# Kernel optimization log

Hardware: AMD Instinct MI355X
Metric: run time of the kernel (lower is better)

The kernel has to match this reference:

```python
import jax, jax.numpy as jnp
import numpy as np

N, E, H, L, T = 20000, 160000, 128, 4, 20


def _ln(x, g, b):
    m = jnp.mean(x, -1, keepdims=True)
    v = jnp.mean((x - m) ** 2, -1, keepdims=True)
    return (x - m) * jax.lax.rsqrt(v + 1e-5) * g + b


def _mlp(x, W1, b1, W2, b2, g, b):
    # Linear -> ReLU -> Linear -> LayerNorm, as in mlp_2layer
    h = jax.nn.relu(x @ W1 + b1)
    return _ln(h @ W2 + b2, g, b)


def setup_inputs() -> dict:
    key = jax.random.key(0)
    ks = iter(jax.random.split(key, 64))

    def W(shape):
        fan_in = shape[-2]
        return jax.random.normal(next(ks), shape, jnp.float32) * (fan_in ** -0.5)

    z = lambda s: jnp.zeros(s, jnp.float32)
    o = lambda s: jnp.ones(s, jnp.float32)

    inp = {
        'x': jax.random.normal(next(ks), (N, 12), jnp.float32),
        'edge_attr': jax.random.normal(next(ks), (E, 4), jnp.float32),
        'edge_index': jax.random.randint(next(ks), (2, E), 0, N),
        # node encoder (12 -> H)
        'Wn1': W((12, H)), 'bn1': z((H,)), 'Wn2': W((H, H)), 'bn2': z((H,)), 'gn_ln': o((H,)), 'bn_ln': z((H,)),
        # edge encoder (4 -> H)
        'We1': W((4, H)), 'be1': z((H,)), 'We2': W((H, H)), 'be2': z((H,)), 'ge_ln': o((H,)), 'be_ln': z((H,)),
        # stacked per-layer params: edge_mlp (4H -> H), node_mlp (3H -> H), global_mlp (3H -> H)
        'lEW1': W((L, 4 * H, H)), 'lEb1': z((L, H)), 'lEW2': W((L, H, H)), 'lEb2': z((L, H)), 'lEg': o((L, H)), 'lEbt': z((L, H)),
        'lVW1': W((L, 3 * H, H)), 'lVb1': z((L, H)), 'lVW2': W((L, H, H)), 'lVb2': z((L, H)), 'lVg': o((L, H)), 'lVbt': z((L, H)),
        'lGW1': W((L, 3 * H, H)), 'lGb1': z((L, H)), 'lGW2': W((L, H, H)), 'lGb2': z((L, H)), 'lGg': o((L, H)), 'lGbt': z((L, H)),
        # CNN output head: Conv1d(1->8,k=15,s=4) -> ReLU -> Conv1d(8->1,k=10,s=1)
        'c1w': jax.random.normal(next(ks), (8, 1, 15), jnp.float32) * 0.1, 'c1b': z((8,)),
        'c2w': jax.random.normal(next(ks), (1, 8, 10), jnp.float32) * 0.1, 'c2b': z((1,)),
    }
    return inp


def _forward(x, edge_attr, edge_index,
             Wn1, bn1, Wn2, bn2, gn_ln, bn_ln,
             We1, be1, We2, be2, ge_ln, be_ln,
             lEW1, lEb1, lEW2, lEb2, lEg, lEbt,
             lVW1, lVb1, lVW2, lVb2, lVg, lVbt,
             lGW1, lGb1, lGW2, lGb2, lGg, lGbt,
             c1w, c1b, c2w, c2b):
    senders = edge_index[0]
    receivers = edge_index[1]
    n_nodes = x.shape[0]
    n_edges = edge_attr.shape[0]

    x_v = _mlp(x, Wn1, bn1, Wn2, bn2, gn_ln, bn_ln)          # [N, H]
    x_e = _mlp(edge_attr, We1, be1, We2, be2, ge_ln, be_ln)  # [E, H]
    g = jnp.zeros((1, H), x_v.dtype)                          # B=1 global (no global inputs)

    def step(carry, p):
        x_v, x_e, g = carry
        (EW1, Eb1, EW2, Eb2, Eg, Ebt,
         VW1, Vb1, VW2, Vb2, Vg, Vbt,
         GW1, Gb1, GW2, Gb2, Gg, Gbt) = p
        # edge update: gather sender/receiver feats, concat with edge + global
        g_e = jnp.broadcast_to(g, (n_edges, H))
        edge_in = jnp.concatenate([x_v[senders], x_v[receivers], x_e, g_e], -1)  # [E, 4H]
        x_e = x_e + _mlp(edge_in, EW1, Eb1, EW2, Eb2, Eg, Ebt)
        # node update: sum-aggregate messages by receiver
        aggr = jax.ops.segment_sum(x_e, receivers, num_segments=n_nodes)  # [N, H]
        g_v = jnp.broadcast_to(g, (n_nodes, H))
        node_in = jnp.concatenate([x_v, aggr, g_v], -1)  # [N, 3H]
        x_v = x_v + _mlp(node_in, VW1, Vb1, VW2, Vb2, Vg, Vbt)
        # global update
        g_in = jnp.concatenate([jnp.sum(x_v, 0, keepdims=True), jnp.sum(x_e, 0, keepdims=True), g], -1)  # [1, 3H]
        g = g + _mlp(g_in, GW1, Gb1, GW2, Gb2, Gg, Gbt)
        return (x_v, x_e, g), None

    params = (lEW1, lEb1, lEW2, lEb2, lEg, lEbt,
              lVW1, lVb1, lVW2, lVb2, lVg, lVbt,
              lGW1, lGb1, lGW2, lGb2, lGg, lGbt)
    (x_v, x_e, g), _ = jax.lax.scan(step, (x_v, x_e, g), params)

    # CNN head over the H=128 feature axis -> [N, T]
    dn = ('NCH', 'OIH', 'NCH')
    h = x_v[:, None, :]  # [N, 1, 128]
    h = jax.lax.conv_general_dilated(h, c1w, (4,), 'VALID', dimension_numbers=dn)
    h = jax.nn.relu(h + c1b[None, :, None])  # [N, 8, 29]
    h = jax.lax.conv_general_dilated(h, c2w, (1,), 'VALID', dimension_numbers=dn) + c2b[None, :, None]
    return h[:, 0, :]  # [N, 20]


def reference(x, edge_attr, edge_index,
              Wn1, bn1, Wn2, bn2, gn_ln, bn_ln,
              We1, be1, We2, be2, ge_ln, be_ln,
              lEW1, lEb1, lEW2, lEb2, lEg, lEbt,
              lVW1, lVb1, lVW2, lVb2, lVg, lVbt,
              lGW1, lGb1, lGW2, lGb2, lGg, lGbt,
              c1w, c1b, c2w, c2b):
    return _forward(x, edge_attr, edge_index,
                    Wn1, bn1, Wn2, bn2, gn_ln, bn_ln,
                    We1, be1, We2, be2, ge_ln, be_ln,
                    lEW1, lEb1, lEW2, lEb2, lEg, lEbt,
                    lVW1, lVb1, lVW2, lVb2, lVg, lVbt,
                    lGW1, lGb1, lGW2, lGb2, lGg, lGbt,
                    c1w, c1b, c2w, c2b)
```

## Files before the change

kernel.cpp:

```cpp
#include <hip/hip_runtime.h>

#define NN 20000
#define NE 160000
#define HD 128
#define SA 136

typedef __attribute__((ext_vector_type(8))) short  bfrag;
typedef __attribute__((ext_vector_type(4))) short  s4v;
typedef __attribute__((ext_vector_type(4))) float  facc;
typedef __attribute__((ext_vector_type(4))) float  f4v;

__device__ __forceinline__ float bf2f(unsigned short u){
  union { unsigned int i; float f; } v; v.i = ((unsigned int)u) << 16; return v.f;
}
__device__ __forceinline__ unsigned short f2bf(float f){
  union { float f; unsigned int i; } v; v.f = f;
  unsigned int r = v.i + 0x7fffu + ((v.i >> 16) & 1u);
  return (unsigned short)(r >> 16);
}

__global__ void sentinel_kernel(float* out, float code){
  if (threadIdx.x < 32) out[threadIdx.x] = code;
}

__device__ __forceinline__ void gemm_tile(const short* Ab,
                                          const unsigned short* pk,
                                          int m0, int lane, facc acc[8]){
  const int q = lane >> 4, c = lane & 15;
  #pragma unroll
  for (int kt = 0; kt < 4; ++kt){
    bfrag a = *(const bfrag*)(Ab + (m0 + c) * SA + kt * 32 + q * 8);
    const bfrag* bp = (const bfrag*)pk + kt * 512 + lane;
    #pragma unroll
    for (int nt = 0; nt < 8; ++nt){
      acc[nt] = __builtin_amdgcn_mfma_f32_16x16x32_bf16(a, bp[nt * 64], acc[nt], 0, 0, 0);
    }
  }
}

__device__ __forceinline__ void gemm_tile_h(const short* Ab,
                                            const unsigned short* pk,
                                            int m0, int ntb, int lane, facc acc[4]){
  const int q = lane >> 4, c = lane & 15;
  #pragma unroll
  for (int kt = 0; kt < 4; ++kt){
    bfrag a = *(const bfrag*)(Ab + (m0 + c) * SA + kt * 32 + q * 8);
    const bfrag* bp = (const bfrag*)pk + kt * 512 + ntb * 64 + lane;
    #pragma unroll
    for (int nt = 0; nt < 4; ++nt){
      acc[nt] = __builtin_amdgcn_mfma_f32_16x16x32_bf16(a, bp[nt * 64], acc[nt], 0, 0, 0);
    }
  }
}

__global__ __launch_bounds__(256) void pack_all(
    const float* Wn2, const float* We2,
    const float* lEW1, const float* lEW2,
    const float* lVW1, const float* lVW2,
    unsigned short* packed)
{
  int job = blockIdx.x * 256 + threadIdx.x;
  int mat = job >> 12, r12 = job & 4095;
  int plane = r12 >> 11, r = r12 & 2047;
  int kt = r >> 9, nt = (r >> 6) & 7, lane = r & 63;
  const float* src;
  if (mat == 0) src = Wn2;
  else if (mat == 1) src = We2;
  else {
    int m2 = mat - 2, l = m2 / 7, t = m2 % 7;
    switch (t){
      case 0: src = lEW1 + ((size_t)l*512 +   0)*HD; break;
      case 1: src = lEW1 + ((size_t)l*512 + 128)*HD; break;
      case 2: src = lEW1 + ((size_t)l*512 + 256)*HD; break;
      case 3: src = lEW2 + (size_t)l*HD*HD;          break;
      case 4: src = lVW1 + ((size_t)l*384 +   0)*HD; break;
      case 5: src = lVW1 + ((size_t)l*384 + 128)*HD; break;
      default: src = lVW2 + (size_t)l*HD*HD;         break;
    }
  }
  int krow = kt*32 + (lane>>4)*8, col = nt*16 + (lane&15);
  unsigned short v[8];
  #pragma unroll
  for (int j = 0; j < 8; ++j){
    float w = src[(size_t)(krow + j)*HD + col];
    unsigned short h = f2bf(w);
    v[j] = plane ? f2bf(w - bf2f(h)) : h;
  }
  unsigned short* dst = packed + ((size_t)mat*2 + plane)*16384
                               + ((size_t)(kt*8+nt)*64 + lane)*8;
  #pragma unroll
  for (int j = 0; j < 8; ++j) dst[j] = v[j];
}

__global__ __launch_bounds__(128) void init_small(
    float* g, float* cbe, float* cbv, float* xvs, float* xes,
    const float* Eb1_0, const float* Vb1_0)
{
  int t = threadIdx.x;
  g[t] = 0.f; xvs[t] = 0.f; xes[t] = 0.f;
  cbe[t] = Eb1_0[t]; cbv[t] = Vb1_0[t];
}

__global__ __launch_bounds__(256) void zero_cnt(int* cnt){
  int i = blockIdx.x * 256 + threadIdx.x;
  if (i < NN) cnt[i] = 0;
}
__global__ __launch_bounds__(256) void hist_kernel(const int* eidx, int* cnt){
  int e = blockIdx.x * 256 + threadIdx.x;
  atomicAdd(&cnt[eidx[NE + e]], 1);
}
__global__ __launch_bounds__(1024) void scan_kernel(const int* cnt, int* base, int* ofs){
  __shared__ int wsum[16];
  int t = threadIdx.x, lane = t & 63;
  int vals[20]; int loc = 0;
  if (t < 1000){
    #pragma unroll
    for (int k = 0; k < 20; ++k){ vals[k] = cnt[t*20 + k]; loc += vals[k]; }
  }
  int inc = loc;
  #pragma unroll
  for (int d = 1; d < 64; d <<= 1){ int o = __shfl_up(inc, d); if (lane >= d) inc += o; }
  if (lane == 63) wsum[t >> 6] = inc;
  __syncthreads();
  if (t < 16){
    int v = wsum[t];
    #pragma unroll
    for (int d = 1; d < 16; d <<= 1){ int o = __shfl_up(v, d); if (t >= d) v += o; }
    wsum[t] = v;
  }
  __syncthreads();
  int woff = (t >= 64) ? wsum[(t >> 6) - 1] : 0;
  int run = woff + inc - loc;
  if (t < 1000){
    #pragma unroll
    for (int k = 0; k < 20; ++k){ base[t*20 + k] = run; ofs[t*20 + k] = run; run += vals[k]; }
  }
  if (t == 0) base[NN] = NE;
}
__global__ __launch_bounds__(256) void scatter_kernel(const int* eidx, int* ofs,
                                                      int* perm, int* ssid, int* srid){
  int e = blockIdx.x * 256 + threadIdx.x;
  int s = eidx[e], r = eidx[NE + e];
  int pos = atomicAdd(&ofs[r], 1);
  perm[pos] = e; ssid[pos] = s; srid[pos] = r;
}

__global__ __launch_bounds__(256) void enc_node(
    const float* x, const float* W1, const float* b1,
    const unsigned short* pkW2, const float* b2,
    const float* gl, const float* bl, float* xvf, int nrows)
{
  __shared__ float inb[64*12];
  __shared__ __align__(16) short Hh[64*SA];
  __shared__ __align__(16) short Hl[64*SA];
  int tid = threadIdx.x, r0 = blockIdx.x * 64;
  for (int j = tid; j < 64*12; j += 256){
    int rr = j / 12, k = j % 12, rg = r0 + rr;
    inb[j] = (rg < nrows) ? x[(size_t)rg*12 + k] : 0.f;
  }
  __syncthreads();
  {
    int cc = tid & 127;
    float w1c[12];
    #pragma unroll
    for (int k = 0; k < 12; ++k) w1c[k] = W1[k*HD + cc];
    float bb = b1[cc];
    for (int it = 0; it < 32; ++it){
      int rr = it*2 + (tid >> 7);
      float a = bb;
      #pragma unroll
      for (int k = 0; k < 12; ++k) a += inb[rr*12 + k] * w1c[k];
      float h = fmaxf(a, 0.f);
      unsigned short hh = f2bf(h);
      Hh[rr*SA + cc] = (short)hh;
      Hl[rr*SA + cc] = (short)f2bf(h - bf2f(hh));
    }
  }
  __syncthreads();
  int lane = tid & 63, q = lane >> 4, c = lane & 15, m0 = (tid >> 6) * 16;
  facc a2[8];
  #pragma unroll
  for (int nt = 0; nt < 8; ++nt) a2[nt] = (facc){0.f,0.f,0.f,0.f};
  gemm_tile(Hh, pkW2,         m0, lane, a2);
  gemm_tile(Hl, pkW2,         m0, lane, a2);
  gemm_tile(Hh, pkW2 + 16384, m0, lane, a2);
  #pragma unroll
  for (int i = 0; i < 4; ++i){
    int rl = m0 + q*4 + i, rg = r0 + rl;
    float vals[8], s = 0.f, ss = 0.f;
    #pragma unroll
    for (int nt = 0; nt < 8; ++nt){
      float v = a2[nt][i] + b2[nt*16 + c];
      vals[nt] = v; s += v; ss += v*v;
    }
    s += __shfl_xor(s,1); ss += __shfl_xor(ss,1);
    s += __shfl_xor(s,2); ss += __shfl_xor(ss,2);
    s += __shfl_xor(s,4); ss += __shfl_xor(ss,4);
    s += __shfl_xor(s,8); ss += __shfl_xor(ss,8);
    float mean = s * 0.0078125f;
    float var  = ss * 0.0078125f - mean*mean;
    float rs   = rsqrtf(var + 1e-5f);
    if (rg < nrows){
      #pragma unroll
      for (int nt = 0; nt < 8; ++nt){
        int col = nt*16 + c;
        xvf[(size_t)rg*HD + col] = (vals[nt]-mean)*rs*gl[col] + bl[col];
      }
    }
  }
}

__global__ __launch_bounds__(256) void enc_edge(
    const float* ea, const int* perm, const float* W1, const float* b1,
    const unsigned short* pkW2, const float* b2,
    const float* gl, const float* bl, unsigned short* xeb)
{
  __shared__ float inb[64*4];
  __shared__ __align__(16) short Hh[64*SA];
  __shared__ __align__(16) short Hl[64*SA];
  int tid = threadIdx.x, r0 = blockIdx.x * 64;
  {
    int rr = tid >> 2, k = tid & 3;
    int pe = perm[r0 + rr];
    inb[tid] = ea[(size_t)pe*4 + k];
  }
  __syncthreads();
  {
    int cc = tid & 127;
    float w0 = W1[0*HD+cc], w1 = W1[1*HD+cc], w2 = W1[2*HD+cc], w3 = W1[3*HD+cc];
    float bb = b1[cc];
    for (int it = 0; it < 32; ++it){
      int rr = it*2 + (tid >> 7);
      float a = bb + inb[rr*4+0]*w0 + inb[rr*4+1]*w1 + inb[rr*4+2]*w2 + inb[rr*4+3]*w3;
      float h = fmaxf(a, 0.f);
      unsigned short hh = f2bf(h);
      Hh[rr*SA + cc] = (short)hh;
      Hl[rr*SA + cc] = (short)f2bf(h - bf2f(hh));
    }
  }
  __syncthreads();
  int lane = tid & 63, q = lane >> 4, c = lane & 15, m0 = (tid >> 6) * 16;
  facc a2[8];
  #pragma unroll
  for (int nt = 0; nt < 8; ++nt) a2[nt] = (facc){0.f,0.f,0.f,0.f};
  gemm_tile(Hh, pkW2,         m0, lane, a2);
  gemm_tile(Hl, pkW2,         m0, lane, a2);
  gemm_tile(Hh, pkW2 + 16384, m0, lane, a2);
  #pragma unroll
  for (int i = 0; i < 4; ++i){
    int rl = m0 + q*4 + i, rg = r0 + rl;
    float vals[8], s = 0.f, ss = 0.f;
    #pragma unroll
    for (int nt = 0; nt < 8; ++nt){
      float v = a2[nt][i] + b2[nt*16 + c];
      vals[nt] = v; s += v; ss += v*v;
    }
    s += __shfl_xor(s,1); ss += __shfl_xor(ss,1);
    s += __shfl_xor(s,2); ss += __shfl_xor(ss,2);
    s += __shfl_xor(s,4); ss += __shfl_xor(ss,4);
    s += __shfl_xor(s,8); ss += __shfl_xor(ss,8);
    float mean = s * 0.0078125f;
    float var  = ss * 0.0078125f - mean*mean;
    float rs   = rsqrtf(var + 1e-5f);
    #pragma unroll
    for (int nt = 0; nt < 8; ++nt){
      int col = nt*16 + c;
      xeb[(size_t)rg*HD + col] = f2bf((vals[nt]-mean)*rs*gl[col] + bl[col]);
    }
  }
}

__global__ __launch_bounds__(512, 4) void pq_kernel(
    const float* xvf, const unsigned short* pkA, const unsigned short* pkB,
    unsigned short* P, unsigned short* Q, int nrows)
{
  __shared__ __align__(16) short Ah[64*SA];
  __shared__ __align__(16) short Al[64*SA];
  int tid = threadIdx.x, r0 = blockIdx.x * 64;
  for (int j = tid; j < 1024; j += 512){
    int rr = j >> 4, ch = j & 15, rg = r0 + rr;
    float v[8];
    if (rg < nrows){
      f4v a = *(const f4v*)(xvf + (size_t)rg*HD + ch*8);
      f4v b = *(const f4v*)(xvf + (size_t)rg*HD + ch*8 + 4);
      v[0]=a[0];v[1]=a[1];v[2]=a[2];v[3]=a[3];v[4]=b[0];v[5]=b[1];v[6]=b[2];v[7]=b[3];
    } else {
      #pragma unroll
      for (int k = 0; k < 8; ++k) v[k] = 0.f;
    }
    short* dh = Ah + rr*SA + ch*8;
    short* dl = Al + rr*SA + ch*8;
    #pragma unroll
    for (int k = 0; k < 8; ++k){
      unsigned short h = f2bf(v[k]);
      dh[k] = (short)h; dl[k] = (short)f2bf(v[k] - bf2f(h));
    }
  }
  __syncthreads();
  int lane = tid & 63, wq = tid >> 6, q = lane >> 4, c = lane & 15;
  int m0 = (wq & 3) * 16, ntb = (wq >> 2) * 4;
  facc ap[4], aq[4];
  #pragma unroll
  for (int nt = 0; nt < 4; ++nt){ ap[nt] = (facc){0.f,0.f,0.f,0.f}; aq[nt] = (facc){0.f,0.f,0.f,0.f}; }
  gemm_tile_h(Ah, pkA,         m0, ntb, lane, ap);
  gemm_tile_h(Al, pkA,         m0, ntb, lane, ap);
  gemm_tile_h(Ah, pkA + 16384, m0, ntb, lane, ap);
  gemm_tile_h(Ah, pkB,         m0, ntb, lane, aq);
  gemm_tile_h(Al, pkB,         m0, ntb, lane, aq);
  gemm_tile_h(Ah, pkB + 16384, m0, ntb, lane, aq);
  #pragma unroll
  for (int i = 0; i < 4; ++i){
    int rl = m0 + q*4 + i, rg = r0 + rl;
    if (rg < nrows){
      s4v pv, qv;
      #pragma unroll
      for (int nt = 0; nt < 4; ++nt){
        pv[nt] = (short)f2bf(ap[nt][i]);
        qv[nt] = (short)f2bf(aq[nt][i]);
      }
      *(s4v*)(P + (size_t)rg*HD + c*8 + ntb) = pv;
      *(s4v*)(Q + (size_t)rg*HD + c*8 + ntb) = qv;
    }
  }
}

__global__ __launch_bounds__(512, 4) void edge_kernel(
    unsigned short* xeb, const int* ssid, const int* srid,
    const unsigned short* P, const unsigned short* Q, const float* cbe,
    const unsigned short* pkW1c, const unsigned short* pkW2,
    const float* Eb2, const float* Eg, const float* Ebt)
{
  __shared__ __align__(16) short Ab[64*SA];
  __shared__ __align__(16) short Hl[64*SA];
  __shared__ float lnS[128], lnSS[128];
  int tid = threadIdx.x, e0 = blockIdx.x * 64;
  int lane = tid & 63, wq = tid >> 6, q = lane >> 4, c = lane & 15;
  int m0 = (wq & 3) * 16, ntb = (wq >> 2) * 4, half = wq >> 2;

  int sid[4], rid[4];
  #pragma unroll
  for (int i = 0; i < 4; ++i){
    int rl = m0 + q*4 + i;
    sid[i] = ssid[e0 + rl];
    rid[i] = srid[e0 + rl];
  }
  s4v psv[4], qrv[4];
  #pragma unroll
  for (int i = 0; i < 4; ++i){
    psv[i] = *(const s4v*)(P + (size_t)sid[i]*HD + c*8 + ntb);
    qrv[i] = *(const s4v*)(Q + (size_t)rid[i]*HD + c*8 + ntb);
  }

  for (int j = tid; j < 1024; j += 512){
    int rr = j >> 4, ch = j & 15;
    *(bfrag*)(Ab + rr*SA + ch*8) = *(const bfrag*)(xeb + (size_t)(e0+rr)*HD + ch*8);
  }
  __syncthreads();

  unsigned int rres[4][2];
  #pragma unroll
  for (int i = 0; i < 4; ++i){
    int rl = m0 + q*4 + i;
    #pragma unroll
    for (int p2 = 0; p2 < 2; ++p2){
      unsigned short a0 = (unsigned short)Ab[rl*SA + (ntb + 2*p2    )*16 + c];
      unsigned short a1 = (unsigned short)Ab[rl*SA + (ntb + 2*p2 + 1)*16 + c];
      rres[i][p2] = ((unsigned int)a1 << 16) | a0;
    }
  }
  float cb[4];
  #pragma unroll
  for (int nt = 0; nt < 4; ++nt) cb[nt] = cbe[(ntb + nt)*16 + c];
  float pg[4][4];
  #pragma unroll
  for (int i = 0; i < 4; ++i){
    #pragma unroll
    for (int nt = 0; nt < 4; ++nt)
      pg[i][nt] = bf2f((unsigned short)psv[i][nt]) + bf2f((unsigned short)qrv[i][nt]) + cb[nt];
  }
  facc acc[4];
  #pragma unroll
  for (int nt = 0; nt < 4; ++nt) acc[nt] = (facc){0.f,0.f,0.f,0.f};
  gemm_tile_h(Ab, pkW1c,         m0, ntb, lane, acc);
  gemm_tile_h(Ab, pkW1c + 16384, m0, ntb, lane, acc);
  __syncthreads();
  #pragma unroll
  for (int i = 0; i < 4; ++i){
    int rl = m0 + q*4 + i;
    #pragma unroll
    for (int nt = 0; nt < 4; ++nt){
      int col = (ntb + nt)*16 + c;
      float h = fmaxf(acc[nt][i] + pg[i][nt], 0.f);
      unsigned short hh = f2bf(h);
      Ab[rl*SA + col] = (short)hh;
      Hl[rl*SA + col] = (short)f2bf(h - bf2f(hh));
    }
  }
  __syncthreads();
  facc a2[4];
  #pragma unroll
  for (int nt = 0; nt < 4; ++nt) a2[nt] = (facc){0.f,0.f,0.f,0.f};
  gemm_tile_h(Ab, pkW2,         m0, ntb, lane, a2);
  gemm_tile_h(Hl, pkW2,         m0, ntb, lane, a2);
  gemm_tile_h(Ab, pkW2 + 16384, m0, ntb, lane, a2);
  float vals[4][4], myS[4], mySS[4];
  #pragma unroll
  for (int i = 0; i < 4; ++i){
    int rl = m0 + q*4 + i;
    float s = 0.f, ss = 0.f;
    #pragma unroll
    for (int nt = 0; nt < 4; ++nt){
      float v = a2[nt][i] + Eb2[(ntb + nt)*16 + c];
      vals[i][nt] = v; s += v; ss += v*v;
    }
    s += __shfl_xor(s,1); ss += __shfl_xor(ss,1);
    s += __shfl_xor(s,2); ss += __shfl_xor(ss,2);
    s += __shfl_xor(s,4); ss += __shfl_xor(ss,4);
    s += __shfl_xor(s,8); ss += __shfl_xor(ss,8);
    myS[i] = s; mySS[i] = ss;
    if (c == 0){ lnS[rl*2 + half] = s; lnSS[rl*2 + half] = ss; }
  }
  __syncthreads();
  #pragma unroll
  for (int i = 0; i < 4; ++i){
    int rl = m0 + q*4 + i, eg = e0 + rl;
    float sT  = myS[i]  + lnS[rl*2 + (half^1)];
    float ssT = mySS[i] + lnSS[rl*2 + (half^1)];
    float mean = sT * 0.0078125f;
    float var  = ssT * 0.0078125f - mean*mean;
    float rs   = rsqrtf(var + 1e-5f);
    #pragma unroll
    for (int nt = 0; nt < 4; ++nt){
      int col = (ntb + nt)*16 + c;
      float o = (vals[i][nt]-mean)*rs*Eg[col] + Ebt[col];
      float rv = bf2f((unsigned short)(rres[i][nt >> 1] >> ((nt & 1)*16)));
      xeb[(size_t)eg*HD + col] = f2bf(rv + o);
    }
  }
}

__global__ __launch_bounds__(512, 4) void node_kernel(
    float* xvf, const unsigned short* xeb, const int* base, const float* cbv,
    const unsigned short* pkW1a, const unsigned short* pkW1b, const unsigned short* pkW2,
    const float* Vb2, const float* Vg, const float* Vbt,
    float* xv_sum, float* xes, int do_xes,
    const unsigned short* pkAn, const unsigned short* pkBn,
    unsigned short* P, unsigned short* Q, int do_pq, int nrows)
{
  __shared__ __align__(16) short Avh[64*SA];
  __shared__ __align__(16) short Avl[64*SA];
  __shared__ __align__(16) short Agh[64*SA];
  __shared__ __align__(16) short Agl[64*SA];
  __shared__ float red[128];
  __shared__ float lnS[128], lnSS[128];
  int tid = threadIdx.x, r0 = blockIdx.x * 64;
  int lane = tid & 63, wq = tid >> 6;
  if (tid < 128) red[tid] = 0.f;
  __syncthreads();
  for (int j = tid; j < 1024; j += 512){
    int rr = j >> 4, ch = j & 15, rg = r0 + rr;
    float v[8];
    if (rg < nrows){
      f4v a = *(const f4v*)(xvf + (size_t)rg*HD + ch*8);
      f4v b = *(const f4v*)(xvf + (size_t)rg*HD + ch*8 + 4);
      v[0]=a[0];v[1]=a[1];v[2]=a[2];v[3]=a[3];v[4]=b[0];v[5]=b[1];v[6]=b[2];v[7]=b[3];
    } else {
      #pragma unroll
      for (int k = 0; k < 8; ++k) v[k] = 0.f;
    }
    short *dvh = Avh + rr*SA + ch*8, *dvl = Avl + rr*SA + ch*8;
    #pragma unroll
    for (int k = 0; k < 8; ++k){
      unsigned short h1 = f2bf(v[k]);
      dvh[k] = (short)h1; dvl[k] = (short)f2bf(v[k] - bf2f(h1));
    }
  }
  float xp0 = 0.f, xp1 = 0.f;
  for (int j = 0; j < 8; ++j){
    int rl = wq*8 + j, rg = r0 + rl;
    float s0 = 0.f, s1 = 0.f;
    if (rg < nrows){
      int b0 = base[rg], b1 = base[rg + 1];
      int e = b0;
      for (; e + 1 < b1; e += 2){
        unsigned int u0 = *(const unsigned int*)(xeb + (size_t)e*HD + lane*2);
        unsigned int u1 = *(const unsigned int*)(xeb + (size_t)(e+1)*HD + lane*2);
        s0 += bf2f((unsigned short)(u0 & 0xffffu)) + bf2f((unsigned short)(u1 & 0xffffu));
        s1 += bf2f((unsigned short)(u0 >> 16))     + bf2f((unsigned short)(u1 >> 16));
      }
      if (e < b1){
        unsigned int u0 = *(const unsigned int*)(xeb + (size_t)e*HD + lane*2);
        s0 += bf2f((unsigned short)(u0 & 0xffffu));
        s1 += bf2f((unsigned short)(u0 >> 16));
      }
    }
    unsigned short h0 = f2bf(s0), h1 = f2bf(s1);
    unsigned short l0 = f2bf(s0 - bf2f(h0)), l1 = f2bf(s1 - bf2f(h1));
    *(unsigned int*)(Agh + rl*SA + 2*lane) = ((unsigned int)h1 << 16) | h0;
    *(unsigned int*)(Agl + rl*SA + 2*lane) = ((unsigned int)l1 << 16) | l0;
    xp0 += s0; xp1 += s1;
  }
  if (do_xes){
    atomicAdd(&red[lane*2],     xp0);
    atomicAdd(&red[lane*2 + 1], xp1);
  }
  __syncthreads();
  if (do_xes && tid < 128) atomicAdd(&xes[tid], red[tid]);
  int q = lane >> 4, c = lane & 15;
  int m0 = (wq & 3) * 16, ntb = (wq >> 2) * 4, half = wq >> 2;
  facc acc[4];
  #pragma unroll
  for (int nt = 0; nt < 4; ++nt) acc[nt] = (facc){0.f,0.f,0.f,0.f};
  gemm_tile_h(Avh, pkW1a,         m0, ntb, lane, acc);
  gemm_tile_h(Avl, pkW1a,         m0, ntb, lane, acc);
  gemm_tile_h(Avh, pkW1a + 16384, m0, ntb, lane, acc);
  gemm_tile_h(Agh, pkW1b,         m0, ntb, lane, acc);
  gemm_tile_h(Agl, pkW1b,         m0, ntb, lane, acc);
  gemm_tile_h(Agh, pkW1b + 16384, m0, ntb, lane, acc);
  __syncthreads();
  #pragma unroll
  for (int i = 0; i < 4; ++i){
    int rl = m0 + q*4 + i;
    #pragma unroll
    for (int nt = 0; nt < 4; ++nt){
      int col = (ntb + nt)*16 + c;
      float h = fmaxf(acc[nt][i] + cbv[col], 0.f);
      unsigned short hh = f2bf(h);
      Avh[rl*SA + col] = (short)hh;
      Avl[rl*SA + col] = (short)f2bf(h - bf2f(hh));
    }
  }
  __syncthreads();
  facc a2[4];
  #pragma unroll
  for (int nt = 0; nt < 4; ++nt) a2[nt] = (facc){0.f,0.f,0.f,0.f};
  gemm_tile_h(Avh, pkW2,         m0, ntb, lane, a2);
  gemm_tile_h(Avl, pkW2,         m0, ntb, lane, a2);
  gemm_tile_h(Avh, pkW2 + 16384, m0, ntb, lane, a2);
  float vals[4][4], myS[4], mySS[4];
  #pragma unroll
  for (int i = 0; i < 4; ++i){
    int rl = m0 + q*4 + i;
    float s = 0.f, ss = 0.f;
    #pragma unroll
    for (int nt = 0; nt < 4; ++nt){
      float v = a2[nt][i] + Vb2[(ntb + nt)*16 + c];
      vals[i][nt] = v; s += v; ss += v*v;
    }
    s += __shfl_xor(s,1); ss += __shfl_xor(ss,1);
    s += __shfl_xor(s,2); ss += __shfl_xor(ss,2);
    s += __shfl_xor(s,4); ss += __shfl_xor(ss,4);
    s += __shfl_xor(s,8); ss += __shfl_xor(ss,8);
    myS[i] = s; mySS[i] = ss;
    if (c == 0){ lnS[rl*2 + half] = s; lnSS[rl*2 + half] = ss; }
  }
  __syncthreads();
  float csum[4] = {0.f,0.f,0.f,0.f};
  #pragma unroll
  for (int i = 0; i < 4; ++i){
    int rl = m0 + q*4 + i, rg = r0 + rl;
    float sT  = myS[i]  + lnS[rl*2 + (half^1)];
    float ssT = mySS[i] + lnSS[rl*2 + (half^1)];
    float mean = sT * 0.0078125f;
    float var  = ssT * 0.0078125f - mean*mean;
    float rs   = rsqrtf(var + 1e-5f);
    if (rg < nrows){
      #pragma unroll
      for (int nt = 0; nt < 4; ++nt){
        int col = (ntb + nt)*16 + c;
        float o = (vals[i][nt]-mean)*rs*Vg[col] + Vbt[col];
        size_t gi = (size_t)rg*HD + col;
        float nv = xvf[gi] + o;
        xvf[gi] = nv;
        csum[nt] += nv;
        if (do_pq){
          unsigned short hh = f2bf(nv);
          Agh[rl*SA + col] = (short)hh;
          Agl[rl*SA + col] = (short)f2bf(nv - bf2f(hh));
        }
      }
    }
  }
  #pragma unroll
  for (int nt = 0; nt < 4; ++nt){
    float v = csum[nt]; v += __shfl_xor(v,16); v += __shfl_xor(v,32);
    if (q == 0) atomicAdd(&xv_sum[(ntb + nt)*16 + c], v);
  }
  if (do_pq){
    __syncthreads();
    facc ap[4], aq[4];
    #pragma unroll
    for (int nt = 0; nt < 4; ++nt){ ap[nt] = (facc){0.f,0.f,0.f,0.f}; aq[nt] = (facc){0.f,0.f,0.f,0.f}; }
    gemm_tile_h(Agh, pkAn,         m0, ntb, lane, ap);
    gemm_tile_h(Agl, pkAn,         m0, ntb, lane, ap);
    gemm_tile_h(Agh, pkAn + 16384, m0, ntb, lane, ap);
    gemm_tile_h(Agh, pkBn,         m0, ntb, lane, aq);
    gemm_tile_h(Agl, pkBn,         m0, ntb, lane, aq);
    gemm_tile_h(Agh, pkBn + 16384, m0, ntb, lane, aq);
    #pragma unroll
    for (int i = 0; i < 4; ++i){
      int rl = m0 + q*4 + i, rg = r0 + rl;
      if (rg < nrows){
        s4v pv, qv;
        #pragma unroll
        for (int nt = 0; nt < 4; ++nt){
          pv[nt] = (short)f2bf(ap[nt][i]);
          qv[nt] = (short)f2bf(aq[nt][i]);
        }
        *(s4v*)(P + (size_t)rg*HD + c*8 + ntb) = pv;
        *(s4v*)(Q + (size_t)rg*HD + c*8 + ntb) = qv;
      }
    }
  }
}

__global__ __launch_bounds__(1024) void g_kernel(
    float* xvs, float* xes, float* g,
    const float* GW1, const float* Gb1, const float* GW2, const float* Gb2,
    const float* Gg, const float* Gbt,
    float* cbe, float* cbv,
    const float* EW1n, const float* Eb1n, const float* VW1n, const float* Vb1n)
{
  __shared__ float gin[384], h1[128], gn[128], red[4];
  __shared__ float partA[8][128], partB[8][128];
  int tid = threadIdx.x, t = tid & 127, kk = tid >> 7;
  if (tid < 384) gin[tid] = (tid < 128) ? xvs[tid] : (tid < 256) ? xes[tid-128] : g[tid-256];
  __syncthreads();
  {
    float a = 0.f;
    for (int k = kk*48; k < kk*48 + 48; ++k) a += gin[k] * GW1[(size_t)k*HD + t];
    partA[kk][t] = a;
  }
  __syncthreads();
  if (kk == 0){
    float a = Gb1[t];
    #pragma unroll
    for (int i = 0; i < 8; ++i) a += partA[i][t];
    h1[t] = fmaxf(a, 0.f);
  }
  __syncthreads();
  {
    float o = 0.f;
    for (int k = kk*16; k < kk*16 + 16; ++k) o += h1[k] * GW2[(size_t)k*HD + t];
    partA[kk][t] = o;
  }
  __syncthreads();
  float oo = 0.f;
  if (kk == 0){
    oo = Gb2[t];
    #pragma unroll
    for (int i = 0; i < 8; ++i) oo += partA[i][t];
  }
  __syncthreads();
  if (tid < 128){
    float s = oo;
    #pragma unroll
    for (int d = 1; d < 64; d <<= 1) s += __shfl_xor(s, d);
    if ((tid & 63) == 0) red[tid >> 6] = s;
  }
  __syncthreads();
  float mean = (red[0] + red[1]) * 0.0078125f;
  if (tid < 128){
    float dd = oo - mean;
    float v = dd * dd;
    #pragma unroll
    for (int d = 1; d < 64; d <<= 1) v += __shfl_xor(v, d);
    if ((tid & 63) == 0) red[2 + (tid >> 6)] = v;
  }
  __syncthreads();
  if (tid < 128){
    float rs = rsqrtf((red[2] + red[3]) * 0.0078125f + 1e-5f);
    float gnv = g[tid] + (oo - mean)*rs*Gg[tid] + Gbt[tid];
    g[tid] = gnv; gn[tid] = gnv;
    xvs[tid] = 0.f; xes[tid] = 0.f;
  }
  __syncthreads();
  {
    float ce = 0.f, cv = 0.f;
    for (int k = kk*16; k < kk*16 + 16; ++k){
      ce += gn[k] * EW1n[(size_t)k*HD + t];
      cv += gn[k] * VW1n[(size_t)k*HD + t];
    }
    partA[kk][t] = ce; partB[kk][t] = cv;
  }
  __syncthreads();
  if (kk == 0){
    float ce = Eb1n[t], cv = Vb1n[t];
    #pragma unroll
    for (int i = 0; i < 8; ++i){ ce += partA[i][t]; cv += partB[i][t]; }
    cbe[t] = ce; cbv[t] = cv;
  }
}

__global__ __launch_bounds__(256) void decoder_kernel(
    const float* xv, const float* c1w, const float* c1b,
    const float* c2w, const float* c2b, float* out)
{
  __shared__ float xl[4][128];
  __shared__ float hl[4][232];
  __shared__ float w1[120], b1[8], w2[80];
  __shared__ float b2s;
  int tid = threadIdx.x, nl = tid >> 6, t = tid & 63;
  int n = blockIdx.x * 4 + nl;
  if (tid < 120) w1[tid] = c1w[tid];
  else if (tid < 128) b1[tid - 120] = c1b[tid - 120];
  else if (tid < 208) w2[tid - 128] = c2w[tid - 128];
  else if (tid == 208) b2s = c2b[0];
  xl[nl][t]      = xv[(size_t)n*HD + t];
  xl[nl][t + 64] = xv[(size_t)n*HD + 64 + t];
  __syncthreads();
  for (int j = t; j < 232; j += 64){
    int ch = j / 29, pp = j % 29;
    float a = b1[ch];
    #pragma unroll
    for (int u = 0; u < 15; ++u) a += xl[nl][4*pp + u] * w1[ch*15 + u];
    hl[nl][j] = fmaxf(a, 0.f);
  }
  __syncthreads();
  if (t < 20){
    float o = b2s;
    #pragma unroll
    for (int ch = 0; ch < 8; ++ch)
      #pragma unroll
      for (int u = 0; u < 10; ++u)
        o += hl[nl][ch*29 + t + u] * w2[ch*10 + u];
    out[(size_t)n*20 + t] = o;
  }
}

extern "C" void kernel_launch(void* const* d_in, const int* in_sizes, int n_in,
                              void* d_out, int out_size, void* d_ws, size_t ws_size,
                              hipStream_t stream)
{
  const float* x    = (const float*)d_in[0];
  const float* ea   = (const float*)d_in[1];
  const int*   eidx = (const int*)d_in[2];
  const float* Wn1  = (const float*)d_in[3];  const float* bn1  = (const float*)d_in[4];
  const float* Wn2  = (const float*)d_in[5];  const float* bn2  = (const float*)d_in[6];
  const float* gnln = (const float*)d_in[7];  const float* bnln = (const float*)d_in[8];
  const float* We1  = (const float*)d_in[9];  const float* be1  = (const float*)d_in[10];
  const float* We2  = (const float*)d_in[11]; const float* be2  = (const float*)d_in[12];
  const float* geln = (const float*)d_in[13]; const float* beln = (const float*)d_in[14];
  const float* lEW1 = (const float*)d_in[15]; const float* lEb1 = (const float*)d_in[16];
  const float* lEW2 = (const float*)d_in[17]; const float* lEb2 = (const float*)d_in[18];
  const float* lEg  = (const float*)d_in[19]; const float* lEbt = (const float*)d_in[20];
  const float* lVW1 = (const float*)d_in[21]; const float* lVb1 = (const float*)d_in[22];
  const float* lVW2 = (const float*)d_in[23]; const float* lVb2 = (const float*)d_in[24];
  const float* lVg  = (const float*)d_in[25]; const float* lVbt = (const float*)d_in[26];
  const float* lGW1 = (const float*)d_in[27]; const float* lGb1 = (const float*)d_in[28];
  const float* lGW2 = (const float*)d_in[29]; const float* lGb2 = (const float*)d_in[30];
  const float* lGg  = (const float*)d_in[31]; const float* lGbt = (const float*)d_in[32];
  const float* c1w  = (const float*)d_in[33]; const float* c1b  = (const float*)d_in[34];
  const float* c2w  = (const float*)d_in[35]; const float* c2b  = (const float*)d_in[36];

  char* ws = (char*)d_ws;
  size_t off = 0;
  auto alloc = [&](size_t b){ size_t o = off; off += (b + 255) & ~(size_t)255; return o; };
  unsigned short* pk   = (unsigned short*)(ws + alloc((size_t)30*2*16384*2));
  float*          g    = (float*)(ws + alloc(512));
  float*          cbe  = (float*)(ws + alloc(512));
  float*          cbv  = (float*)(ws + alloc(512));
  float*          xvs  = (float*)(ws + alloc(512));
  float*          xes  = (float*)(ws + alloc(512));
  float*          xvf  = (float*)(ws + alloc((size_t)NN*HD*4));
  unsigned short* P    = (unsigned short*)(ws + alloc((size_t)NN*HD*2));
  unsigned short* Q    = (unsigned short*)(ws + alloc((size_t)NN*HD*2));
  unsigned short* xeb  = (unsigned short*)(ws + alloc((size_t)NE*HD*2));
  int*            cnt  = (int*)(ws + alloc((size_t)NN*4));
  int*            bse  = (int*)(ws + alloc((size_t)(NN+1)*4));
  int*            ofs  = (int*)(ws + alloc((size_t)NN*4));
  int*            perm = (int*)(ws + alloc((size_t)NE*4));
  int*            ssid = (int*)(ws + alloc((size_t)NE*4));
  int*            srid = (int*)(ws + alloc((size_t)NE*4));

  if (ws_size < off){
    sentinel_kernel<<<1, 32, 0, stream>>>((float*)d_out, 20000.f + (float)(ws_size >> 20));
    return;
  }

  auto slot = [&](int m){ return pk + (size_t)m * 32768; };

  pack_all<<<480, 256, 0, stream>>>(Wn2, We2, lEW1, lEW2, lVW1, lVW2, pk);
  init_small<<<1, 128, 0, stream>>>(g, cbe, cbv, xvs, xes, lEb1, lVb1);
  zero_cnt<<<(NN + 255)/256, 256, 0, stream>>>(cnt);
  hist_kernel<<<NE/256, 256, 0, stream>>>(eidx, cnt);
  scan_kernel<<<1, 1024, 0, stream>>>(cnt, bse, ofs);
  scatter_kernel<<<NE/256, 256, 0, stream>>>(eidx, ofs, perm, ssid, srid);

  enc_node<<<(NN + 63)/64, 256, 0, stream>>>(x, Wn1, bn1, slot(0), bn2, gnln, bnln, xvf, NN);
  enc_edge<<<NE/64, 256, 0, stream>>>(ea, perm, We1, be1, slot(1), be2, geln, beln, xeb);

  pq_kernel<<<(NN + 63)/64, 512, 0, stream>>>(xvf, slot(2), slot(3), P, Q, NN);

  for (int l = 0; l < 4; ++l){
    int m = 2 + 7*l;
    edge_kernel<<<NE/64, 512, 0, stream>>>(xeb, ssid, srid, P, Q, cbe,
        slot(m+2), slot(m+3),
        lEb2 + (size_t)l*HD, lEg + (size_t)l*HD, lEbt + (size_t)l*HD);
    node_kernel<<<(NN + 63)/64, 512, 0, stream>>>(xvf, xeb, bse, cbv,
        slot(m+4), slot(m+5), slot(m+6),
        lVb2 + (size_t)l*HD, lVg + (size_t)l*HD, lVbt + (size_t)l*HD,
        xvs, xes, (l < 3) ? 1 : 0,
        slot(m+7), slot(m+8), P, Q, (l < 3) ? 1 : 0, NN);
    if (l < 3){
      g_kernel<<<1, 1024, 0, stream>>>(xvs, xes, g,
          lGW1 + (size_t)l*384*HD, lGb1 + (size_t)l*HD,
          lGW2 + (size_t)l*HD*HD, lGb2 + (size_t)l*HD,
          lGg + (size_t)l*HD, lGbt + (size_t)l*HD,
          cbe, cbv,
          lEW1 + ((size_t)(l+1)*512 + 384)*HD, lEb1 + (size_t)(l+1)*HD,
          lVW1 + ((size_t)(l+1)*384 + 256)*HD, lVb1 + (size_t)(l+1)*HD);
    }
  }
  decoder_kernel<<<NN/4, 256, 0, stream>>>(xvf, c1w, c1b, c2w, c2b, (float*)d_out);

  hipError_t e = hipGetLastError();
  if (e != hipSuccess){
    sentinel_kernel<<<1, 32, 0, stream>>>((float*)d_out, 10000.f + (float)e);
  }
  (void)in_sizes; (void)n_in; (void)out_size;
}
```

Measured before the change: 832.7 us.

## Double node_kernel block to 1024 threads, splitting GEMM columns across 16 waves

The node kernel now launches 1024 threads per 64-row block instead of 512. Each wave handles a 16x32 output tile instead of 16x64, and the edge-aggregation loop gives each wave 4 rows instead of 8. LayerNorm partial sums are now combined across four column groups through shared memory. This adds parallelism to the node stage and shortens each wave's serial gather and GEMM work, at the cost of more barriers, larger blocks, and possibly lower occupancy per CU.

```diff
diff --git a/kernel.cpp b/kernel.cpp
--- a/kernel.cpp
+++ b/kernel.cpp
@@ -48,6 +48,21 @@
     const bfrag* bp = (const bfrag*)pk + kt * 512 + ntb * 64 + lane;
     #pragma unroll
     for (int nt = 0; nt < 4; ++nt){
+      acc[nt] = __builtin_amdgcn_mfma_f32_16x16x32_bf16(a, bp[nt * 64], acc[nt], 0, 0, 0);
+    }
+  }
+}
+
+__device__ __forceinline__ void gemm_tile_q(const short* Ab,
+                                            const unsigned short* pk,
+                                            int m0, int ntb, int lane, facc acc[2]){
+  const int q = lane >> 4, c = lane & 15;
+  #pragma unroll
+  for (int kt = 0; kt < 4; ++kt){
+    bfrag a = *(const bfrag*)(Ab + (m0 + c) * SA + kt * 32 + q * 8);
+    const bfrag* bp = (const bfrag*)pk + kt * 512 + ntb * 64 + lane;
+    #pragma unroll
+    for (int nt = 0; nt < 2; ++nt){
       acc[nt] = __builtin_amdgcn_mfma_f32_16x16x32_bf16(a, bp[nt * 64], acc[nt], 0, 0, 0);
     }
   }
@@ -439,7 +454,7 @@
   }
 }
 
-__global__ __launch_bounds__(512, 4) void node_kernel(
+__global__ __launch_bounds__(1024, 4) void node_kernel(
     float* xvf, const unsigned short* xeb, const int* base, const float* cbv,
     const unsigned short* pkW1a, const unsigned short* pkW1b, const unsigned short* pkW2,
     const float* Vb2, const float* Vg, const float* Vbt,
@@ -452,12 +467,13 @@
   __shared__ __align__(16) short Agh[64*SA];
   __shared__ __align__(16) short Agl[64*SA];
   __shared__ float red[128];
-  __shared__ float lnS[128], lnSS[128];
+  __shared__ float lnS[256], lnSS[256];
   int tid = threadIdx.x, r0 = blockIdx.x * 64;
   int lane = tid & 63, wq = tid >> 6;
   if (tid < 128) red[tid] = 0.f;
   __syncthreads();
-  for (int j = tid; j < 1024; j += 512){
+  {
+    int j = tid;
     int rr = j >> 4, ch = j & 15, rg = r0 + rr;
     float v[8];
     if (rg < nrows){
@@ -476,8 +492,8 @@
     }
   }
   float xp0 = 0.f, xp1 = 0.f;
-  for (int j = 0; j < 8; ++j){
-    int rl = wq*8 + j, rg = r0 + rl;
+  for (int j = 0; j < 4; ++j){
+    int rl = wq*4 + j, rg = r0 + rl;
     float s0 = 0.f, s1 = 0.f;
     if (rg < nrows){
       int b0 = base[rg], b1 = base[rg + 1];
@@ -507,22 +523,22 @@
   __syncthreads();
   if (do_xes && tid < 128) atomicAdd(&xes[tid], red[tid]);
   int q = lane >> 4, c = lane & 15;
-  int m0 = (wq & 3) * 16, ntb = (wq >> 2) * 4, half = wq >> 2;
-  facc acc[4];
-  #pragma unroll
-  for (int nt = 0; nt < 4; ++nt) acc[nt] = (facc){0.f,0.f,0.f,0.f};
-  gemm_tile_h(Avh, pkW1a,         m0, ntb, lane, acc);
-  gemm_tile_h(Avl, pkW1a,         m0, ntb, lane, acc);
-  gemm_tile_h(Avh, pkW1a + 16384, m0, ntb, lane, acc);
-  gemm_tile_h(Agh, pkW1b,         m0, ntb, lane, acc);
-  gemm_tile_h(Agl, pkW1b,         m0, ntb, lane, acc);
-  gemm_tile_h(Agh, pkW1b + 16384, m0, ntb, lane, acc);
+  int m0 = (wq & 3) * 16, ntb = (wq >> 2) * 2, cg = wq >> 2;
+  facc acc[2];
+  #pragma unroll
+  for (int nt = 0; nt < 2; ++nt) acc[nt] = (facc){0.f,0.f,0.f,0.f};
+  gemm_tile_q(Avh, pkW1a,         m0, ntb, lane, acc);
+  gemm_tile_q(Avl, pkW1a,         m0, ntb, lane, acc);
+  gemm_tile_q(Avh, pkW1a + 16384, m0, ntb, lane, acc);
+  gemm_tile_q(Agh, pkW1b,         m0, ntb, lane, acc);
+  gemm_tile_q(Agl, pkW1b,         m0, ntb, lane, acc);
+  gemm_tile_q(Agh, pkW1b + 16384, m0, ntb, lane, acc);
   __syncthreads();
   #pragma unroll
   for (int i = 0; i < 4; ++i){
     int rl = m0 + q*4 + i;
     #pragma unroll
-    for (int nt = 0; nt < 4; ++nt){
+    for (int nt = 0; nt < 2; ++nt){
       int col = (ntb + nt)*16 + c;
       float h = fmaxf(acc[nt][i] + cbv[col], 0.f);
       unsigned short hh = f2bf(h);
@@ -531,19 +547,19 @@
     }
   }
   __syncthreads();
-  facc a2[4];
-  #pragma unroll
-  for (int nt = 0; nt < 4; ++nt) a2[nt] = (facc){0.f,0.f,0.f,0.f};
-  gemm_tile_h(Avh, pkW2,         m0, ntb, lane, a2);
-  gemm_tile_h(Avl, pkW2,         m0, ntb, lane, a2);
-  gemm_tile_h(Avh, pkW2 + 16384, m0, ntb, lane, a2);
-  float vals[4][4], myS[4], mySS[4];
+  facc a2[2];
+  #pragma unroll
+  for (int nt = 0; nt < 2; ++nt) a2[nt] = (facc){0.f,0.f,0.f,0.f};
+  gemm_tile_q(Avh, pkW2,         m0, ntb, lane, a2);
+  gemm_tile_q(Avl, pkW2,         m0, ntb, lane, a2);
+  gemm_tile_q(Avh, pkW2 + 16384, m0, ntb, lane, a2);
+  float vals[4][2];
   #pragma unroll
   for (int i = 0; i < 4; ++i){
     int rl = m0 + q*4 + i;
     float s = 0.f, ss = 0.f;
     #pragma unroll
-    for (int nt = 0; nt < 4; ++nt){
+    for (int nt = 0; nt < 2; ++nt){
       float v = a2[nt][i] + Vb2[(ntb + nt)*16 + c];
       vals[i][nt] = v; s += v; ss += v*v;
     }
@@ -551,22 +567,21 @@
     s += __shfl_xor(s,2); ss += __shfl_xor(ss,2);
     s += __shfl_xor(s,4); ss += __shfl_xor(ss,4);
     s += __shfl_xor(s,8); ss += __shfl_xor(ss,8);
-    myS[i] = s; mySS[i] = ss;
-    if (c == 0){ lnS[rl*2 + half] = s; lnSS[rl*2 + half] = ss; }
-  }
-  __syncthreads();
-  float csum[4] = {0.f,0.f,0.f,0.f};
+    if (c == 0){ lnS[rl*4 + cg] = s; lnSS[rl*4 + cg] = ss; }
+  }
+  __syncthreads();
+  float csum[2] = {0.f,0.f};
   #pragma unroll
   for (int i = 0; i < 4; ++i){
     int rl = m0 + q*4 + i, rg = r0 + rl;
-    float sT  = myS[i]  + lnS[rl*2 + (half^1)];
-    float ssT = mySS[i] + lnSS[rl*2 + (half^1)];
+    float sT  = (lnS[rl*4+0]  + lnS[rl*4+1])  + (lnS[rl*4+2]  + lnS[rl*4+3]);
+    float ssT = (lnSS[rl*4+0] + lnSS[rl*4+1]) + (lnSS[rl*4+2] + lnSS[rl*4+3]);
     float mean = sT * 0.0078125f;
     float var  = ssT * 0.0078125f - mean*mean;
     float rs   = rsqrtf(var + 1e-5f);
     if (rg < nrows){
       #pragma unroll
-      for (int nt = 0; nt < 4; ++nt){
+      for (int nt = 0; nt < 2; ++nt){
         int col = (ntb + nt)*16 + c;
         float o = (vals[i][nt]-mean)*rs*Vg[col] + Vbt[col];
         size_t gi = (size_t)rg*HD + col;
@@ -582,33 +597,29 @@
     }
   }
   #pragma unroll
-  for (int nt = 0; nt < 4; ++nt){
+  for (int nt = 0; nt < 2; ++nt){
     float v = csum[nt]; v += __shfl_xor(v,16); v += __shfl_xor(v,32);
     if (q == 0) atomicAdd(&xv_sum[(ntb + nt)*16 + c], v);
   }
   if (do_pq){
     __syncthreads();
-    facc ap[4], aq[4];
-    #pragma unroll
-    for (int nt = 0; nt < 4; ++nt){ ap[nt] = (facc){0.f,0.f,0.f,0.f}; aq[nt] = (facc){0.f,0.f,0.f,0.f}; }
-    gemm_tile_h(Agh, pkAn,         m0, ntb, lane, ap);
-    gemm_tile_h(Agl, pkAn,         m0, ntb, lane, ap);
-    gemm_tile_h(Agh, pkAn + 16384, m0, ntb, lane, ap);
-    gemm_tile_h(Agh, pkBn,         m0, ntb, lane, aq);
-    gemm_tile_h(Agl, pkBn,         m0, ntb, lane, aq);
-    gemm_tile_h(Agh, pkBn + 16384, m0, ntb, lane, aq);
+    facc ap[2], aq[2];
+    #pragma unroll
+    for (int nt = 0; nt < 2; ++nt){ ap[nt] = (facc){0.f,0.f,0.f,0.f}; aq[nt] = (facc){0.f,0.f,0.f,0.f}; }
+    gemm_tile_q(Agh, pkAn,         m0, ntb, lane, ap);
+    gemm_tile_q(Agl, pkAn,         m0, ntb, lane, ap);
+    gemm_tile_q(Agh, pkAn + 16384, m0, ntb, lane, ap);
+    gemm_tile_q(Agh, pkBn,         m0, ntb, lane, aq);
+    gemm_tile_q(Agl, pkBn,         m0, ntb, lane, aq);
+    gemm_tile_q(Agh, pkBn + 16384, m0, ntb, lane, aq);
     #pragma unroll
     for (int i = 0; i < 4; ++i){
       int rl = m0 + q*4 + i, rg = r0 + rl;
       if (rg < nrows){
-        s4v pv, qv;
-        #pragma unroll
-        for (int nt = 0; nt < 4; ++nt){
-          pv[nt] = (short)f2bf(ap[nt][i]);
-          qv[nt] = (short)f2bf(aq[nt][i]);
-        }
-        *(s4v*)(P + (size_t)rg*HD + c*8 + ntb) = pv;
-        *(s4v*)(Q + (size_t)rg*HD + c*8 + ntb) = qv;
+        unsigned int pv = ((unsigned int)f2bf(ap[1][i]) << 16) | f2bf(ap[0][i]);
+        unsigned int qv = ((unsigned int)f2bf(aq[1][i]) << 16) | f2bf(aq[0][i]);
+        *(unsigned int*)(P + (size_t)rg*HD + c*8 + ntb) = pv;
+        *(unsigned int*)(Q + (size_t)rg*HD + c*8 + ntb) = qv;
       }
     }
   }
@@ -797,7 +808,7 @@
     edge_kernel<<<NE/64, 512, 0, stream>>>(xeb, ssid, srid, P, Q, cbe,
         slot(m+2), slot(m+3),
         lEb2 + (size_t)l*HD, lEg + (size_t)l*HD, lEbt + (size_t)l*HD);
-    node_kernel<<<(NN + 63)/64, 512, 0, stream>>>(xvf, xeb, bse, cbv,
+    node_kernel<<<(NN + 63)/64, 1024, 0, stream>>>(xvf, xeb, bse, cbv,
         slot(m+4), slot(m+5), slot(m+6),
         lVb2 + (size_t)l*HD, lVg + (size_t)l*HD, lVbt + (size_t)l*HD,
         xvs, xes, (l < 3) ? 1 : 0,
```

After: 854.9 us. 2.7% more time.
